# Kernel tuning notes

Hardware: AMD Instinct MI355X
Metric: run time of the kernel (lower is better)

## Reference

```python
import jax, jax.numpy as jnp
import numpy as np

EMBED = 768
HEADS = 12
HEAD_DIM = EMBED // HEADS
HIDDEN = 4 * EMBED
EPS = 1e-5


def _layernorm(x, w, b):
    mu = jnp.mean(x, axis=-1, keepdims=True)
    var = jnp.mean(jnp.square(x - mu), axis=-1, keepdims=True)
    return (x - mu) * jax.lax.rsqrt(var + EPS) * w + b


def setup_inputs() -> dict:
    key = jax.random.key(0)
    ks = jax.random.split(key, 12)
    s = 0.02
    return {
        "x": jax.random.normal(ks[0], (2, 2048, EMBED), dtype=jnp.float32),
        "ln1_w": jnp.ones((EMBED,), jnp.float32),
        "ln1_b": jnp.zeros((EMBED,), jnp.float32),
        "qkv_w": jax.random.normal(ks[1], (3 * EMBED, EMBED), jnp.float32) * s,
        "qkv_b": jnp.zeros((3 * EMBED,), jnp.float32),
        "proj_w": jax.random.normal(ks[2], (EMBED, EMBED), jnp.float32) * s,
        "proj_b": jnp.zeros((EMBED,), jnp.float32),
        "ln2_w": jnp.ones((EMBED,), jnp.float32),
        "ln2_b": jnp.zeros((EMBED,), jnp.float32),
        "fc1_w": jax.random.normal(ks[3], (HIDDEN, EMBED), jnp.float32) * s,
        "fc1_b": jnp.zeros((HIDDEN,), jnp.float32),
        "fc2_w": jax.random.normal(ks[4], (EMBED, HIDDEN), jnp.float32) * s,
        "fc2_b": jnp.zeros((EMBED,), jnp.float32),
    }


def reference(x, ln1_w, ln1_b, qkv_w, qkv_b, proj_w, proj_b,
              ln2_w, ln2_b, fc1_w, fc1_b, fc2_w, fc2_b):
    B, N, C = x.shape
    scale = float(HEAD_DIM) ** 0.5  # NOTE: module MULTIPLIES by sqrt(head_dim)

    # --- attention branch ---
    h = _layernorm(x, ln1_w, ln1_b)
    qkv = h @ qkv_w.T + qkv_b                     # [B,N,3C]
    qkv = qkv.reshape(B, N, 3, HEADS, HEAD_DIM)
    q = qkv[:, :, 0].transpose(0, 2, 1, 3)        # [B,H,N,D]
    k = qkv[:, :, 1].transpose(0, 2, 1, 3)
    v = qkv[:, :, 2].transpose(0, 2, 1, 3)
    attn = jnp.einsum('bhnd,bhmd->bhnm', q, k) * scale
    attn = jax.nn.softmax(attn, axis=-1)
    o = jnp.einsum('bhnm,bhmd->bhnd', attn, v)    # [B,H,N,D]
    o = o.transpose(0, 2, 1, 3).reshape(B, N, C)
    x = x + (o @ proj_w.T + proj_b)

    # --- MLP branch ---
    h = _layernorm(x, ln2_w, ln2_b)
    h = jax.nn.gelu(h @ fc1_w.T + fc1_b, approximate=False)
    x = x + (h @ fc2_w.T + fc2_b)
    return x
```

## Files before the change

### kernel.cpp

```cpp
#include <hip/hip_runtime.h>
#include <hip/hip_bf16.h>

typedef __attribute__((ext_vector_type(8))) short short8;
typedef __attribute__((ext_vector_type(4))) float f32x4;
typedef __attribute__((ext_vector_type(2))) int i32x2;
typedef __attribute__((ext_vector_type(4))) int i32x4;

__device__ inline unsigned short f2bs(float f) {
  union { float f; unsigned u; } v; v.f = f;
  unsigned r = v.u + 0x7fff + ((v.u >> 16) & 1);
  return (unsigned short)(r >> 16);
}

__device__ inline unsigned pkbf(float a, float b) {
  __hip_bfloat162 h = __float22bfloat162_rn(float2{a, b});
  union { __hip_bfloat162 h; unsigned u; } c; c.h = h;
  return c.u;
}

__device__ inline void gload16(const void* g, void* l) {
  __builtin_amdgcn_global_load_lds((const __attribute__((address_space(1))) void*)g,
                                   (__attribute__((address_space(3))) void*)l,
                                   16, 0, 0);
}

__global__ void cvt_bf16(const float* __restrict__ in, unsigned short* __restrict__ out, int n4) {
  int i = blockIdx.x * blockDim.x + threadIdx.x;
  if (i >= n4) return;
  float4 v = ((const float4*)in)[i];
  ushort4 o;
  o.x = f2bs(v.x); o.y = f2bs(v.y); o.z = f2bs(v.z); o.w = f2bs(v.w);
  ((ushort4*)out)[i] = o;
}

__global__ __launch_bounds__(256)
void ln_kernel(const float* __restrict__ x, const float* __restrict__ w,
               const float* __restrict__ bsh, unsigned short* __restrict__ out)
{
  const int row = blockIdx.x;
  const float* xr = x + (size_t)row * 768;
  float v[3];
  float s = 0.f, sq = 0.f;
#pragma unroll
  for (int i = 0; i < 3; ++i) {
    v[i] = xr[threadIdx.x + i * 256];
    s += v[i]; sq += v[i] * v[i];
  }
#pragma unroll
  for (int d = 1; d < 64; d <<= 1) {
    s  += __shfl_xor(s, d, 64);
    sq += __shfl_xor(sq, d, 64);
  }
  __shared__ float ss[4], ssq[4];
  const int wv = threadIdx.x >> 6;
  if ((threadIdx.x & 63) == 0) { ss[wv] = s; ssq[wv] = sq; }
  __syncthreads();
  s  = ss[0] + ss[1] + ss[2] + ss[3];
  sq = ssq[0] + ssq[1] + ssq[2] + ssq[3];
  const float mu = s * (1.0f / 768.0f);
  const float var = sq * (1.0f / 768.0f) - mu * mu;
  const float rstd = rsqrtf(var + 1e-5f);
#pragma unroll
  for (int i = 0; i < 3; ++i) {
    const int c = threadIdx.x + i * 256;
    out[(size_t)row * 768 + c] = f2bs((v[i] - mu) * rstd * w[c] + bsh[c]);
  }
}

template<int S>
__global__ __launch_bounds__(256)
void reduce_k(const float* __restrict__ p, const float* __restrict__ bias,
              const float* __restrict__ resid, float* __restrict__ out)
{
  const size_t MN = 4096ull * 768;
  const size_t i = ((size_t)blockIdx.x * 256 + threadIdx.x) * 4;
  float4 a = *(const float4*)(p + i);
#pragma unroll
  for (int s = 1; s < S; ++s) {
    float4 b = *(const float4*)(p + s * MN + i);
    a.x += b.x; a.y += b.y; a.z += b.z; a.w += b.w;
  }
  const int col = (int)(i % 768);
  float4 bb = *(const float4*)(bias + col);
  float4 rr = *(const float4*)(resid + i);
  a.x += bb.x + rr.x; a.y += bb.y + rr.y; a.z += bb.z + rr.z; a.w += bb.w + rr.w;
  *(float4*)(out + i) = a;
}

template<int EPI>
__global__ __launch_bounds__(256, 3)
void gemm_nt(const unsigned short* __restrict__ A,
             const unsigned short* __restrict__ Bw,
             const float* __restrict__ bias,
             const float* __restrict__ resid,
             void* __restrict__ out0, void* __restrict__ out1, void* __restrict__ out2,
             int M, int N, int Kslice, int Kstride)
{
  __shared__ __align__(16) unsigned short As[3][128 * 32];
  __shared__ __align__(16) unsigned short Bs[3][128 * 32];
  const int tid = threadIdx.x;
  const int lane = tid & 63;
  const int w = tid >> 6;
  const int wr = w >> 1, wc = w & 1;
  const int l15 = lane & 15, g = lane >> 4;

  const int nwg = gridDim.x * gridDim.y;
  const int hw = blockIdx.y * gridDim.x + blockIdx.x;
  const int virt = (hw & 7) * (nwg >> 3) + (hw >> 3);
  const int m0 = (virt / gridDim.x) * 128;
  const int n0 = (virt % gridDim.x) * 128;
  const int kbase = blockIdx.z * Kslice;

  f32x4 acc[4][4];
#pragma unroll
  for (int m = 0; m < 4; ++m)
#pragma unroll
    for (int n = 0; n < 4; ++n)
      acc[m][n] = (f32x4){0.f, 0.f, 0.f, 0.f};

  auto stage = [&](int buf, int k0) {
#pragma unroll
    for (int i = 0; i < 2; ++i) {
      const int f = tid + i * 256;
      const int row = f >> 2, c8 = f & 3;
      const int sc = c8 ^ (row & 3);
      gload16(A  + (size_t)(m0 + row) * Kstride + kbase + k0 + sc * 8, (char*)&As[buf][0] + f * 16);
      gload16(Bw + (size_t)(n0 + row) * Kstride + kbase + k0 + sc * 8, (char*)&Bs[buf][0] + f * 16);
    }
  };

  const int NT = Kslice >> 5;
  stage(0, 0);
  stage(1, 32);

  for (int t = 0; t < NT; ++t) {
    const int buf = t % 3;
    if (t + 2 < NT) {
      stage((t + 2) % 3, (t + 2) * 32);
      asm volatile("s_waitcnt vmcnt(8)" ::: "memory");
    } else if (t + 1 < NT) {
      asm volatile("s_waitcnt vmcnt(4)" ::: "memory");
    } else {
      asm volatile("s_waitcnt vmcnt(0)" ::: "memory");
    }
    __builtin_amdgcn_s_barrier();
    asm volatile("" ::: "memory");

    short8 af[4], bfr[4];
#pragma unroll
    for (int m = 0; m < 4; ++m) {
      const int r = wr * 64 + m * 16 + l15;
      af[m] = *(const short8*)((const char*)&As[buf][0] + ((size_t)r * 32 + (g ^ (r & 3)) * 8) * 2);
    }
#pragma unroll
    for (int n = 0; n < 4; ++n) {
      const int r = wc * 64 + n * 16 + l15;
      bfr[n] = *(const short8*)((const char*)&Bs[buf][0] + ((size_t)r * 32 + (g ^ (r & 3)) * 8) * 2);
    }
#pragma unroll
    for (int m = 0; m < 4; ++m)
#pragma unroll
      for (int n = 0; n < 4; ++n)
        acc[m][n] = __builtin_amdgcn_mfma_f32_16x16x32_bf16(af[m], bfr[n], acc[m][n], 0, 0, 0);

    asm volatile("" ::: "memory");
    __builtin_amdgcn_s_barrier();
  }

#pragma unroll
  for (int m = 0; m < 4; ++m) {
    const int gmBase = m0 + wr * 64 + m * 16 + g * 4;
#pragma unroll
    for (int n = 0; n < 4; ++n) {
      const int gn = n0 + wc * 64 + n * 16 + l15;
      const float bval = (EPI == 4) ? 0.0f : bias[gn];
      float vj[4];
#pragma unroll
      for (int j = 0; j < 4; ++j) vj[j] = acc[m][n][j] + bval;
      if (EPI == 0) {
        const int three = gn / 768;
        const int hh = (gn % 768) >> 6;
        const int d = gn & 63;
        const int bb = gmBase >> 11, t = gmBase & 2047;
        if (three == 2) {
          ushort4 pk;
          pk.x = f2bs(vj[0]); pk.y = f2bs(vj[1]); pk.z = f2bs(vj[2]); pk.w = f2bs(vj[3]);
          *(ushort4*)((unsigned short*)out2 + (((size_t)bb * 12 + hh) * 64 + d) * 2048 + t) = pk;
        } else {
          unsigned short* dst = (three == 0) ? (unsigned short*)out0 : (unsigned short*)out1;
#pragma unroll
          for (int j = 0; j < 4; ++j) {
            float v = vj[j];
            if (three == 0) v *= 8.0f;
            dst[(((size_t)bb * 12 + hh) * 2048 + (t + j)) * 64 + d] = f2bs(v);
          }
        }
      } else if (EPI == 1 || EPI == 3) {
#pragma unroll
        for (int j = 0; j < 4; ++j) {
          const int gm = gmBase + j;
          ((float*)out0)[(size_t)gm * N + gn] = vj[j] + resid[(size_t)gm * N + gn];
        }
      } else if (EPI == 2) {
#pragma unroll
        for (int j = 0; j < 4; ++j) {
          const int gm = gmBase + j;
          const float ge = 0.5f * vj[j] * (1.0f + erff(vj[j] * 0.70710678f));
          ((unsigned short*)out0)[(size_t)gm * N + gn] = f2bs(ge);
        }
      } else {
        float* po = (float*)out0 + (size_t)blockIdx.z * M * N;
#pragma unroll
        for (int j = 0; j < 4; ++j) {
          const int gm = gmBase + j;
          po[(size_t)gm * N + gn] = vj[j];
        }
      }
    }
  }
}

__global__ __launch_bounds__(256, 4)
void attn_fwd(const unsigned short* __restrict__ Q,
              const unsigned short* __restrict__ K,
              const unsigned short* __restrict__ Vt,
              unsigned short* __restrict__ O)
{
  __shared__ __align__(1024) unsigned short Ks[2][8 * 512];
  __shared__ __align__(1024) unsigned short Vs[2][4096];
  const int tid = threadIdx.x, lane = tid & 63, w = tid >> 6;
  const int l15 = lane & 15, g = lane >> 4;

  const int hw = blockIdx.y * gridDim.x + blockIdx.x;
  const int virt = (hw & 7) * 96 + (hw >> 3);
  const int qblk = virt & 31;
  const int bh = virt >> 5;
  const int b = bh / 12, h = bh % 12;
  const int q0 = qblk * 64;
  const unsigned short* Qb = Q  + (size_t)bh * 2048 * 64;
  const unsigned short* Kb = K  + (size_t)bh * 2048 * 64;
  const unsigned short* Vb = Vt + (size_t)bh * 64 * 2048;

  const int qr = q0 + w * 16 + l15;
  short8 qf[2];
  qf[0] = *(const short8*)(Qb + (size_t)qr * 64 + g * 8);
  qf[1] = *(const short8*)(Qb + (size_t)qr * 64 + 32 + g * 8);

  float m_run = -1e30f, l_run = 0.f;
  f32x4 o_acc[4];
#pragma unroll
  for (int dc = 0; dc < 4; ++dc) o_acc[dc] = (f32x4){0.f, 0.f, 0.f, 0.f};

  const int vtok = ((lane & 7) ^ (lane >> 3)) * 8;

  auto stage = [&](int buf, int kb) {
#pragma unroll
    for (int i = 0; i < 2; ++i) {
      const int f = w * 2 + i;
      const int n = f >> 1, kc = f & 1;
      gload16(Kb + (size_t)(kb + n * 16 + l15) * 64 + kc * 32 + g * 8,
              (char*)&Ks[buf][0] + f * 1024);
    }
#pragma unroll
    for (int i = 0; i < 2; ++i) {
      const int c = w * 2 + i;
      const int d = c * 8 + (lane >> 3);
      gload16(Vb + (size_t)d * 2048 + kb + vtok,
              (char*)&Vs[buf][0] + c * 1024);
    }
  };

  stage(0, 0);
  __syncthreads();
  int cur = 0;

  for (int t = 0; t < 32; ++t) {
    if (t < 31) {
      stage(cur ^ 1, (t + 1) * 64);
      asm volatile("s_waitcnt vmcnt(4)" ::: "memory");
    } else {
      asm volatile("s_waitcnt vmcnt(0)" ::: "memory");
    }
    __builtin_amdgcn_s_barrier();
    asm volatile("" ::: "memory");

    f32x4 s2[4];
#pragma unroll
    for (int n = 0; n < 4; ++n) s2[n] = (f32x4){0.f, 0.f, 0.f, 0.f};
    __builtin_amdgcn_s_setprio(1);
#pragma unroll
    for (int n = 0; n < 4; ++n) {
      short8 kf0 = *(const short8*)(&Ks[cur][(n * 2 + 0) * 512 + lane * 8]);
      short8 kf1 = *(const short8*)(&Ks[cur][(n * 2 + 1) * 512 + lane * 8]);
      s2[n] = __builtin_amdgcn_mfma_f32_16x16x32_bf16(kf0, qf[0], s2[n], 0, 0, 0);
      s2[n] = __builtin_amdgcn_mfma_f32_16x16x32_bf16(kf1, qf[1], s2[n], 0, 0, 0);
    }
    __builtin_amdgcn_s_setprio(0);

    float mx = s2[0][0];
#pragma unroll
    for (int n = 0; n < 4; ++n)
#pragma unroll
      for (int j = 0; j < 4; ++j) mx = fmaxf(mx, s2[n][j]);
    mx = fmaxf(mx, __shfl_xor(mx, 16, 64));
    mx = fmaxf(mx, __shfl_xor(mx, 32, 64));
    if (__any(mx > m_run)) {
      const float mn = fmaxf(m_run, mx);
      const float alpha = __expf(m_run - mn);
      m_run = mn;
      l_run *= alpha;
#pragma unroll
      for (int j = 0; j < 4; ++j) {
        const float aB = __shfl(alpha, (lane & 48) | (g * 4 + j), 64);
#pragma unroll
        for (int dc = 0; dc < 4; ++dc) o_acc[dc][j] *= aB;
      }
    }
    float e[4][4];
    float rs = 0.f;
#pragma unroll
    for (int n = 0; n < 4; ++n)
#pragma unroll
      for (int j = 0; j < 4; ++j) {
        e[n][j] = __expf(s2[n][j] - m_run);
        rs += e[n][j];
      }
    rs += __shfl_xor(rs, 16, 64);
    rs += __shfl_xor(rs, 32, 64);
    l_run += rs;

    unsigned pw[2][4];
#pragma unroll
    for (int kc = 0; kc < 2; ++kc) {
      pw[kc][0] = pkbf(e[2 * kc][0],     e[2 * kc][1]);
      pw[kc][1] = pkbf(e[2 * kc][2],     e[2 * kc][3]);
      pw[kc][2] = pkbf(e[2 * kc + 1][0], e[2 * kc + 1][1]);
      pw[kc][3] = pkbf(e[2 * kc + 1][2], e[2 * kc + 1][3]);
    }

    const char* vsb = (const char*)&Vs[cur][0];
    const unsigned sw = (unsigned)(l15 & 7) << 4;
#pragma unroll
    for (int kc = 0; kc < 2; ++kc) {
      i32x4 pt; pt.x = (int)pw[kc][0]; pt.y = (int)pw[kc][1]; pt.z = (int)pw[kc][2]; pt.w = (int)pw[kc][3];
      short8 pf = *(short8*)&pt;
      __builtin_amdgcn_s_setprio(1);
#pragma unroll
      for (int dc = 0; dc < 4; ++dc) {
        const unsigned row = (unsigned)(dc * 16 + l15) * 128;
        i32x2 ra  = *(const i32x2*)(vsb + row + (((unsigned)(kc * 64 + g * 8)) ^ sw));
        i32x2 rb2 = *(const i32x2*)(vsb + row + (((unsigned)(kc * 64 + 32 + g * 8)) ^ sw));
        i32x4 vt4; vt4.x = ra.x; vt4.y = ra.y; vt4.z = rb2.x; vt4.w = rb2.y;
        short8 vf = *(short8*)&vt4;
        o_acc[dc] = __builtin_amdgcn_mfma_f32_16x16x32_bf16(pf, vf, o_acc[dc], 0, 0, 0);
      }
      __builtin_amdgcn_s_setprio(0);
    }

    asm volatile("" ::: "memory");
    __builtin_amdgcn_s_barrier();
    cur ^= 1;
  }

#pragma unroll
  for (int j = 0; j < 4; ++j) {
    const float lB = __shfl(l_run, (lane & 48) | (g * 4 + j), 64);
    const float inv = 1.0f / lB;
    const int qrow = q0 + w * 16 + g * 4 + j;
#pragma unroll
    for (int dc = 0; dc < 4; ++dc) {
      O[((size_t)b * 2048 + qrow) * 768 + h * 64 + dc * 16 + l15] = f2bs(o_acc[dc][j] * inv);
    }
  }
}

extern "C" void kernel_launch(void* const* d_in, const int* in_sizes, int n_in,
                              void* d_out, int out_size, void* d_ws, size_t ws_size,
                              hipStream_t stream)
{
  const float* x      = (const float*)d_in[0];
  const float* ln1_w  = (const float*)d_in[1];
  const float* ln1_b  = (const float*)d_in[2];
  const float* qkv_w  = (const float*)d_in[3];
  const float* qkv_b  = (const float*)d_in[4];
  const float* proj_w = (const float*)d_in[5];
  const float* proj_b = (const float*)d_in[6];
  const float* ln2_w  = (const float*)d_in[7];
  const float* ln2_b  = (const float*)d_in[8];
  const float* fc1_w  = (const float*)d_in[9];
  const float* fc1_b  = (const float*)d_in[10];
  const float* fc2_w  = (const float*)d_in[11];
  const float* fc2_b  = (const float*)d_in[12];

  char* base = (char*)d_ws;
  size_t off = 0;
  auto take = [&](size_t bytes) {
    void* r = base + off;
    off = (off + bytes + 255) & ~(size_t)255;
    return r;
  };
  unsigned short* wq = (unsigned short*)take(2304ull * 768 * 2);
  unsigned short* wp = (unsigned short*)take(768ull * 768 * 2);
  unsigned short* w1 = (unsigned short*)take(3072ull * 768 * 2);
  unsigned short* w2 = (unsigned short*)take(768ull * 3072 * 2);
  unsigned short* h  = (unsigned short*)take(4096ull * 768 * 2);
  float* x2          = (float*)take(4096ull * 768 * 4);
  char* big          = (char*)take(4096ull * 3072 * 2);
  unsigned short* Qb = (unsigned short*)big;
  unsigned short* Kb = (unsigned short*)(big + 4096ull * 768 * 2);
  unsigned short* Vb = (unsigned short*)(big + 2ull * 4096 * 768 * 2);
  unsigned short* a2 = (unsigned short*)big;
  float* part        = (float*)take(4ull * 4096 * 768 * 4);
  const bool can_split = off <= ws_size;

  int n4;
  n4 = 2304 * 768 / 4; cvt_bf16<<<(n4 + 255) / 256, 256, 0, stream>>>(qkv_w, wq, n4);
  n4 = 768 * 768 / 4;  cvt_bf16<<<(n4 + 255) / 256, 256, 0, stream>>>(proj_w, wp, n4);
  n4 = 3072 * 768 / 4; cvt_bf16<<<(n4 + 255) / 256, 256, 0, stream>>>(fc1_w, w1, n4);
  n4 = 768 * 3072 / 4; cvt_bf16<<<(n4 + 255) / 256, 256, 0, stream>>>(fc2_w, w2, n4);

  ln_kernel<<<4096, 256, 0, stream>>>(x, ln1_w, ln1_b, h);
  gemm_nt<0><<<dim3(18, 32), 256, 0, stream>>>(h, wq, qkv_b, nullptr, Qb, Kb, Vb, 4096, 2304, 768, 768);
  attn_fwd<<<dim3(32, 24), 256, 0, stream>>>(Qb, Kb, Vb, h);

  if (can_split) {
    gemm_nt<4><<<dim3(6, 32, 2), 256, 0, stream>>>(h, wp, nullptr, nullptr, part, nullptr, nullptr, 4096, 768, 384, 768);
    reduce_k<2><<<3072, 256, 0, stream>>>(part, proj_b, x, x2);
  } else {
    gemm_nt<1><<<dim3(6, 32), 256, 0, stream>>>(h, wp, proj_b, x, x2, nullptr, nullptr, 4096, 768, 768, 768);
  }

  ln_kernel<<<4096, 256, 0, stream>>>(x2, ln2_w, ln2_b, h);
  gemm_nt<2><<<dim3(24, 32), 256, 0, stream>>>(h, w1, fc1_b, nullptr, a2, nullptr, nullptr, 4096, 3072, 768, 768);

  if (can_split) {
    gemm_nt<4><<<dim3(6, 32, 4), 256, 0, stream>>>(a2, w2, nullptr, nullptr, part, nullptr, nullptr, 4096, 768, 768, 3072);
    reduce_k<4><<<3072, 256, 0, stream>>>(part, fc2_b, x2, (float*)d_out);
  } else {
    gemm_nt<3><<<dim3(6, 32), 256, 0, stream>>>(a2, w2, fc2_b, x2, d_out, nullptr, nullptr, 4096, 768, 3072, 3072);
  }
}
```

Baseline: 213.0 us.

## Triple-buffer attention, pre-swizzle V layout, use exp2, drop trailing barriers

The GEMM and attention loops now issue the next-next stage after the top barrier and drop the end-of-iteration barrier, which a three-buffer ring makes safe. The QKV epilogue writes V in an MFMA-fragment-ready tiled layout so attention reads V with one 16-byte LDS load per fragment instead of two swizzled 8-byte loads. Q is prescaled by sqrt(64)*log2(e) so softmax can use the raw v_exp_f32 (exp2), and the row-sum shuffle reduction moves out of the loop to the end. Attention occupancy drops from 4 to 3 blocks per CU because of the larger LDS footprint.

```diff
diff --git a/kernel.cpp b/kernel.cpp
--- a/kernel.cpp
+++ b/kernel.cpp
@@ -3,7 +3,6 @@
 
 typedef __attribute__((ext_vector_type(8))) short short8;
 typedef __attribute__((ext_vector_type(4))) float f32x4;
-typedef __attribute__((ext_vector_type(2))) int i32x2;
 typedef __attribute__((ext_vector_type(4))) int i32x4;
 
 __device__ inline unsigned short f2bs(float f) {
@@ -16,6 +15,10 @@
   __hip_bfloat162 h = __float22bfloat162_rn(float2{a, b});
   union { __hip_bfloat162 h; unsigned u; } c; c.h = h;
   return c.u;
+}
+
+__device__ inline float exp2v(float x) {
+  float r; asm("v_exp_f32 %0, %1" : "=v"(r) : "v"(x)); return r;
 }
 
 __device__ inline void gload16(const void* g, void* l) {
@@ -135,16 +138,14 @@
 
   for (int t = 0; t < NT; ++t) {
     const int buf = t % 3;
-    if (t + 2 < NT) {
-      stage((t + 2) % 3, (t + 2) * 32);
-      asm volatile("s_waitcnt vmcnt(8)" ::: "memory");
-    } else if (t + 1 < NT) {
+    if (t + 1 < NT) {
       asm volatile("s_waitcnt vmcnt(4)" ::: "memory");
     } else {
       asm volatile("s_waitcnt vmcnt(0)" ::: "memory");
     }
     __builtin_amdgcn_s_barrier();
     asm volatile("" ::: "memory");
+    if (t + 2 < NT) stage((t + 2) % 3, (t + 2) * 32);
 
     short8 af[4], bfr[4];
 #pragma unroll
@@ -162,9 +163,7 @@
 #pragma unroll
       for (int n = 0; n < 4; ++n)
         acc[m][n] = __builtin_amdgcn_mfma_f32_16x16x32_bf16(af[m], bfr[n], acc[m][n], 0, 0, 0);
-
     asm volatile("" ::: "memory");
-    __builtin_amdgcn_s_barrier();
   }
 
 #pragma unroll
@@ -185,13 +184,16 @@
         if (three == 2) {
           ushort4 pk;
           pk.x = f2bs(vj[0]); pk.y = f2bs(vj[1]); pk.z = f2bs(vj[2]); pk.w = f2bs(vj[3]);
-          *(ushort4*)((unsigned short*)out2 + (((size_t)bb * 12 + hh) * 64 + d) * 2048 + t) = pk;
+          const int kt = t & 63;
+          const size_t pos = ((((size_t)(bb * 12 + hh) * 32 + (t >> 6)) * 8 + (d >> 4) * 2 + (kt >> 5)) * 64
+                              + ((kt >> 2) & 3) * 16 + (d & 15)) * 8 + ((kt >> 4) & 1) * 4;
+          *(ushort4*)((unsigned short*)out2 + pos) = pk;
         } else {
           unsigned short* dst = (three == 0) ? (unsigned short*)out0 : (unsigned short*)out1;
 #pragma unroll
           for (int j = 0; j < 4; ++j) {
             float v = vj[j];
-            if (three == 0) v *= 8.0f;
+            if (three == 0) v *= 11.5415603f;
             dst[(((size_t)bb * 12 + hh) * 2048 + (t + j)) * 64 + d] = f2bs(v);
           }
         }
@@ -220,14 +222,14 @@
   }
 }
 
-__global__ __launch_bounds__(256, 4)
+__global__ __launch_bounds__(256, 3)
 void attn_fwd(const unsigned short* __restrict__ Q,
               const unsigned short* __restrict__ K,
-              const unsigned short* __restrict__ Vt,
+              const unsigned short* __restrict__ Vf,
               unsigned short* __restrict__ O)
 {
-  __shared__ __align__(1024) unsigned short Ks[2][8 * 512];
-  __shared__ __align__(1024) unsigned short Vs[2][4096];
+  __shared__ __align__(1024) unsigned short Ks[3][4096];
+  __shared__ __align__(1024) unsigned short Vs[3][4096];
   const int tid = threadIdx.x, lane = tid & 63, w = tid >> 6;
   const int l15 = lane & 15, g = lane >> 4;
 
@@ -239,21 +241,20 @@
   const int q0 = qblk * 64;
   const unsigned short* Qb = Q  + (size_t)bh * 2048 * 64;
   const unsigned short* Kb = K  + (size_t)bh * 2048 * 64;
-  const unsigned short* Vb = Vt + (size_t)bh * 64 * 2048;
+  const unsigned short* Vb = Vf + (size_t)bh * 2048 * 64;
 
   const int qr = q0 + w * 16 + l15;
   short8 qf[2];
   qf[0] = *(const short8*)(Qb + (size_t)qr * 64 + g * 8);
   qf[1] = *(const short8*)(Qb + (size_t)qr * 64 + 32 + g * 8);
 
-  float m_run = -1e30f, l_run = 0.f;
+  float m_run = -1e30f, l_part = 0.f;
   f32x4 o_acc[4];
 #pragma unroll
   for (int dc = 0; dc < 4; ++dc) o_acc[dc] = (f32x4){0.f, 0.f, 0.f, 0.f};
 
-  const int vtok = ((lane & 7) ^ (lane >> 3)) * 8;
-
-  auto stage = [&](int buf, int kb) {
+  auto stage = [&](int buf, int tIdx) {
+    const int kb = tIdx * 64;
 #pragma unroll
     for (int i = 0; i < 2; ++i) {
       const int f = w * 2 + i;
@@ -263,26 +264,25 @@
     }
 #pragma unroll
     for (int i = 0; i < 2; ++i) {
-      const int c = w * 2 + i;
-      const int d = c * 8 + (lane >> 3);
-      gload16(Vb + (size_t)d * 2048 + kb + vtok,
-              (char*)&Vs[buf][0] + c * 1024);
+      const int chunk = tid + i * 256;
+      gload16(Vb + (size_t)tIdx * 4096 + chunk * 8,
+              (char*)&Vs[buf][0] + chunk * 16);
     }
   };
 
   stage(0, 0);
-  __syncthreads();
-  int cur = 0;
+  stage(1, 1);
 
   for (int t = 0; t < 32; ++t) {
+    const int buf = t % 3;
     if (t < 31) {
-      stage(cur ^ 1, (t + 1) * 64);
       asm volatile("s_waitcnt vmcnt(4)" ::: "memory");
     } else {
       asm volatile("s_waitcnt vmcnt(0)" ::: "memory");
     }
     __builtin_amdgcn_s_barrier();
     asm volatile("" ::: "memory");
+    if (t < 30) stage((t + 2) % 3, t + 2);
 
     f32x4 s2[4];
 #pragma unroll
@@ -290,8 +290,8 @@
     __builtin_amdgcn_s_setprio(1);
 #pragma unroll
     for (int n = 0; n < 4; ++n) {
-      short8 kf0 = *(const short8*)(&Ks[cur][(n * 2 + 0) * 512 + lane * 8]);
-      short8 kf1 = *(const short8*)(&Ks[cur][(n * 2 + 1) * 512 + lane * 8]);
+      short8 kf0 = *(const short8*)(&Ks[buf][(n * 2 + 0) * 512 + lane * 8]);
+      short8 kf1 = *(const short8*)(&Ks[buf][(n * 2 + 1) * 512 + lane * 8]);
       s2[n] = __builtin_amdgcn_mfma_f32_16x16x32_bf16(kf0, qf[0], s2[n], 0, 0, 0);
       s2[n] = __builtin_amdgcn_mfma_f32_16x16x32_bf16(kf1, qf[1], s2[n], 0, 0, 0);
     }
@@ -306,9 +306,9 @@
     mx = fmaxf(mx, __shfl_xor(mx, 32, 64));
     if (__any(mx > m_run)) {
       const float mn = fmaxf(m_run, mx);
-      const float alpha = __expf(m_run - mn);
+      const float alpha = exp2v(m_run - mn);
       m_run = mn;
-      l_run *= alpha;
+      l_part *= alpha;
 #pragma unroll
       for (int j = 0; j < 4; ++j) {
         const float aB = __shfl(alpha, (lane & 48) | (g * 4 + j), 64);
@@ -322,12 +322,10 @@
     for (int n = 0; n < 4; ++n)
 #pragma unroll
       for (int j = 0; j < 4; ++j) {
-        e[n][j] = __expf(s2[n][j] - m_run);
+        e[n][j] = exp2v(s2[n][j] - m_run);
         rs += e[n][j];
       }
-    rs += __shfl_xor(rs, 16, 64);
-    rs += __shfl_xor(rs, 32, 64);
-    l_run += rs;
+    l_part += rs;
 
     unsigned pw[2][4];
 #pragma unroll
@@ -338,33 +336,27 @@
       pw[kc][3] = pkbf(e[2 * kc + 1][2], e[2 * kc + 1][3]);
     }
 
-    const char* vsb = (const char*)&Vs[cur][0];
-    const unsigned sw = (unsigned)(l15 & 7) << 4;
+    const char* vsb = (const char*)&Vs[buf][0];
+    __builtin_amdgcn_s_setprio(1);
 #pragma unroll
     for (int kc = 0; kc < 2; ++kc) {
       i32x4 pt; pt.x = (int)pw[kc][0]; pt.y = (int)pw[kc][1]; pt.z = (int)pw[kc][2]; pt.w = (int)pw[kc][3];
       short8 pf = *(short8*)&pt;
-      __builtin_amdgcn_s_setprio(1);
 #pragma unroll
       for (int dc = 0; dc < 4; ++dc) {
-        const unsigned row = (unsigned)(dc * 16 + l15) * 128;
-        i32x2 ra  = *(const i32x2*)(vsb + row + (((unsigned)(kc * 64 + g * 8)) ^ sw));
-        i32x2 rb2 = *(const i32x2*)(vsb + row + (((unsigned)(kc * 64 + 32 + g * 8)) ^ sw));
-        i32x4 vt4; vt4.x = ra.x; vt4.y = ra.y; vt4.z = rb2.x; vt4.w = rb2.y;
-        short8 vf = *(short8*)&vt4;
-        o_acc[dc] = __builtin_amdgcn_mfma_f32_16x16x32_bf16(pf, vf, o_acc[dc], 0, 0, 0);
+        short8 vfr = *(const short8*)(vsb + (((dc * 2 + kc) * 64 + lane) * 16));
+        o_acc[dc] = __builtin_amdgcn_mfma_f32_16x16x32_bf16(pf, vfr, o_acc[dc], 0, 0, 0);
       }
-      __builtin_amdgcn_s_setprio(0);
-    }
-
+    }
+    __builtin_amdgcn_s_setprio(0);
     asm volatile("" ::: "memory");
-    __builtin_amdgcn_s_barrier();
-    cur ^= 1;
-  }
-
+  }
+
+  l_part += __shfl_xor(l_part, 16, 64);
+  l_part += __shfl_xor(l_part, 32, 64);
 #pragma unroll
   for (int j = 0; j < 4; ++j) {
-    const float lB = __shfl(l_run, (lane & 48) | (g * 4 + j), 64);
+    const float lB = __shfl(l_part, (lane & 48) | (g * 4 + j), 64);
     const float inv = 1.0f / lB;
     const int qrow = q0 + w * 16 + g * 4 + j;
 #pragma unroll
```

After: 207.0 us. 2.8% less time.
